# Performance work log

Hardware: AMD Instinct MI355X
Metric: run time of the kernel (lower is better)

Reference implementation:

```python
import jax, jax.numpy as jnp
import numpy as np

H = 16        # attention heads
KVH = 4       # kv heads (GQA)
D = 128       # qk head_dim = qk_nope(64) + qk_rope(64)
ROPE = 64     # rotary sub-dim
VCH = 128     # v_channels
HID = 2048    # hidden size
E = 8         # routed experts
K = 2         # top-k
EPS = 1e-6
THETA = 10000.0


def rmsnorm(x, w):
    return x * jax.lax.rsqrt(jnp.mean(x * x, axis=-1, keepdims=True) + EPS) * w


def apply_rope(x, pos):
    # x: [T, h, ROPE]; rotate-half convention on the rope sub-dim
    half = ROPE // 2
    inv_freq = 1.0 / (THETA ** (jnp.arange(half, dtype=jnp.float32) / half))
    ang = pos.astype(jnp.float32)[:, None] * inv_freq          # [T, half]
    cos = jnp.cos(ang)[:, None, :]
    sin = jnp.sin(ang)[:, None, :]
    x1, x2 = x[..., :half], x[..., half:]
    return jnp.concatenate([x1 * cos - x2 * sin, x1 * sin + x2 * cos], axis=-1)


def swiglu(x, w_gate, w_up, w_down):
    return (jax.nn.silu(x @ w_gate) * (x @ w_up)) @ w_down


def setup_inputs() -> dict:
    key = jax.random.key(0)
    ks = jax.random.split(key, 16)
    T = 2048
    sc = 0.02
    n = lambda k, s: jax.random.normal(k, s, dtype=jnp.float32) * sc
    return {
        "x": jax.random.normal(ks[0], (T, HID), dtype=jnp.float32),
        "positions": jnp.arange(T, dtype=jnp.int32),
        "ln1_w": jnp.ones((HID,), jnp.float32),
        "qkv_w": n(ks[1], (HID, H * D + KVH * D + KVH * VCH)),
        "qkv_b": n(ks[2], (H * D + KVH * D + KVH * VCH,)),
        "k_ln_w": jnp.ones((D,), jnp.float32),
        "o_w": n(ks[3], (H * VCH, HID)),
        "ln2_w": jnp.ones((HID,), jnp.float32),
        "router_w": n(ks[4], (HID, E)),
        "w1": n(ks[5], (E, HID, 512)),
        "w2": n(ks[6], (E, 512, HID)),
        "w3": n(ks[7], (E, HID, 512)),
        "sw1": n(ks[8], (HID, 1024)),
        "sw2": n(ks[9], (1024, HID)),
        "sw3": n(ks[10], (HID, 1024)),
    }


def reference(x, positions, ln1_w, qkv_w, qkv_b, k_ln_w, o_w, ln2_w,
              router_w, w1, w2, w3, sw1, sw2, sw3):
    T = x.shape[0]
    # --- attention block ---
    h = rmsnorm(x, ln1_w)
    qkv = h @ qkv_w + qkv_b
    q = qkv[:, : H * D].reshape(T, H, D)
    k = qkv[:, H * D : H * D + KVH * D].reshape(T, KVH, D)
    v = qkv[:, H * D + KVH * D :].reshape(T, KVH, VCH)
    k = rmsnorm(k, k_ln_w)  # per-head k_layernorm over head_dim
    # rope applied to the trailing qk_rope_dim of q/k
    q = jnp.concatenate([q[..., : D - ROPE], apply_rope(q[..., D - ROPE :], positions)], -1)
    k = jnp.concatenate([k[..., : D - ROPE], apply_rope(k[..., D - ROPE :], positions)], -1)
    rep = H // KVH
    kf = jnp.repeat(k, rep, axis=1)   # [T, H, D]
    vf = jnp.repeat(v, rep, axis=1)   # [T, H, VCH]
    scale = D ** -0.5
    scores = jnp.einsum("qhd,khd->hqk", q, kf) * scale
    causal = jnp.tril(jnp.ones((T, T), dtype=bool))
    scores = jnp.where(causal[None], scores, jnp.float32(-1e30))
    p = jax.nn.softmax(scores, axis=-1)
    attn = jnp.einsum("hqk,khv->qhv", p, vf).reshape(T, H * VCH)
    x = x + attn @ o_w
    # --- MoE block: shared expert + top-k routed experts ---
    h2 = rmsnorm(x, ln2_w)
    probs = jax.nn.softmax(h2 @ router_w, axis=-1)            # [T, E]
    topw, topi = jax.lax.top_k(probs, K)
    topw = topw / jnp.sum(topw, axis=-1, keepdims=True)        # renormalize top-k
    combine = jnp.sum(jax.nn.one_hot(topi, E, dtype=h2.dtype) * topw[..., None], axis=1)  # [T, E]
    moe = swiglu(h2, sw1, sw3, sw2)                            # shared expert
    for e in range(E):  # small fixed expert count
        moe = moe + combine[:, e : e + 1] * swiglu(h2, w1[e], w3[e], w2[e])
    return x + moe
```

## Files before the change

### kernel.cpp

```cpp
#include <hip/hip_runtime.h>


typedef _Float16 half_t;
typedef _Float16 half8 __attribute__((ext_vector_type(8)));
typedef _Float16 half2v __attribute__((ext_vector_type(2)));
typedef float    f32x4 __attribute__((ext_vector_type(4)));
typedef float    floatx4 __attribute__((ext_vector_type(4)));

#define T_TOK 2048
#define HIDN  2048
#define NH    16
#define NKVH  4
#define HD    128
#define QKV_N 3072
#define NEXP  8
#define NPAIR_MAX 4608

#define MFMA16(a,b,c) __builtin_amdgcn_mfma_f32_16x16x32_f16(a,b,c,0,0,0)

__device__ __forceinline__ void gload_lds16(const half_t* g, half_t* l) {
    __builtin_amdgcn_global_load_lds(
        (const __attribute__((address_space(1))) void*)g,
        (__attribute__((address_space(3))) void*)l, 16, 0, 0);
}

__device__ __forceinline__ float silu_f(float g) {
    return g / (1.0f + expf(-g));
}

__global__ __launch_bounds__(256)
void rmsnorm_split_k(const float* __restrict__ x, const float* __restrict__ w,
                     half_t* __restrict__ hi, half_t* __restrict__ lo)
{
    const int row = blockIdx.x, tid = threadIdx.x;
    const float* xr = x + (size_t)row * HIDN;
    floatx4 v0 = *(const floatx4*)(xr + tid * 8);
    floatx4 v1 = *(const floatx4*)(xr + tid * 8 + 4);
    float ss = v0[0]*v0[0] + v0[1]*v0[1] + v0[2]*v0[2] + v0[3]*v0[3]
             + v1[0]*v1[0] + v1[1]*v1[1] + v1[2]*v1[2] + v1[3]*v1[3];
    for (int o = 32; o; o >>= 1) ss += __shfl_down(ss, o);
    __shared__ float red[4];
    if ((tid & 63) == 0) red[tid >> 6] = ss;
    __syncthreads();
    ss = red[0] + red[1] + red[2] + red[3];
    float rs = rsqrtf(ss * (1.0f / HIDN) + 1e-6f);
    floatx4 w0 = *(const floatx4*)(w + tid * 8);
    floatx4 w1 = *(const floatx4*)(w + tid * 8 + 4);
    float vv[8] = { v0[0]*w0[0], v0[1]*w0[1], v0[2]*w0[2], v0[3]*w0[3],
                    v1[0]*w1[0], v1[1]*w1[1], v1[2]*w1[2], v1[3]*w1[3] };
    half8 hv, lv;
#pragma unroll
    for (int j = 0; j < 8; ++j) {
        float o = vv[j] * rs;
        half_t h = (half_t)o;
        hv[j] = h;
        lv[j] = (half_t)((o - (float)h) * 1024.0f);
    }
    *(half8*)(hi + (size_t)row * HIDN + tid * 8) = hv;
    if (lo) *(half8*)(lo + (size_t)row * HIDN + tid * 8) = lv;
}

__global__ __launch_bounds__(256)
void transpose_split2(const float* __restrict__ src,
                      half_t* __restrict__ dh, half_t* __restrict__ dl,
                      int sstride, int dstride)
{
    __shared__ float tile[32][36];
    const int n0 = blockIdx.x * 32, k0 = blockIdx.y * 32;
    const int tid = threadIdx.x;
    {
        int r = tid >> 3, c = (tid & 7) * 4;
        *(floatx4*)&tile[r][c] =
            *(const floatx4*)(src + (size_t)(k0 + r) * sstride + n0 + c);
    }
    __syncthreads();
    int n = tid & 31, g = tid >> 5, gg = g & 3;
    half8 hv;
    if (g < 4) {
#pragma unroll
        for (int j = 0; j < 8; ++j) hv[j] = (half_t)tile[gg * 8 + j][n];
        *(half8*)(dh + (size_t)(n0 + n) * dstride + k0 + gg * 8) = hv;
    } else {
#pragma unroll
        for (int j = 0; j < 8; ++j) {
            float v = tile[gg * 8 + j][n];
            half_t h = (half_t)v;
            hv[j] = (half_t)((v - (float)h) * 1024.0f);
        }
        *(half8*)(dl + (size_t)(n0 + n) * dstride + k0 + gg * 8) = hv;
    }
}

__global__ __launch_bounds__(256)
void transpose_f16(const float* __restrict__ src, half_t* __restrict__ dh,
                   int sstride, int dstride)
{
    __shared__ float tile[32][68];
    const int n0 = blockIdx.x * 64, k0 = blockIdx.y * 32;
    const int tid = threadIdx.x;
    {
        int r = tid >> 3, c = (tid & 7) * 4;
        const float* s = src + (size_t)(k0 + r) * sstride + n0;
        *(floatx4*)&tile[r][c]      = *(const floatx4*)(s + c);
        *(floatx4*)&tile[r][c + 32] = *(const floatx4*)(s + c + 32);
    }
    __syncthreads();
    int n = tid & 63, g = tid >> 6;
    half8 hv;
#pragma unroll
    for (int j = 0; j < 8; ++j) hv[j] = (half_t)tile[g * 8 + j][n];
    *(half8*)(dh + (size_t)(n0 + n) * dstride + k0 + g * 8) = hv;
}

__global__ __launch_bounds__(256)
void vt_transpose_perm(const float* __restrict__ src, half_t* __restrict__ dh)
{
    __shared__ float tile[32][68];
    const int n0 = blockIdx.x * 64, k0 = blockIdx.y * 32;
    const int tid = threadIdx.x;
    {
        int r = tid >> 3, c = (tid & 7) * 4;
        const float* s = src + (size_t)(k0 + r) * QKV_N + n0;
        *(floatx4*)&tile[r][c]      = *(const floatx4*)(s + c);
        *(floatx4*)&tile[r][c + 32] = *(const floatx4*)(s + c + 32);
    }
    __syncthreads();
    int n = tid & 63, g = tid >> 6;
    half8 hv;
#pragma unroll
    for (int tt = 0; tt < 8; ++tt) {
        int c_src = (tt & 1) * 16 + 4 * g + (tt >> 1);
        hv[tt] = (half_t)tile[c_src][n];
    }
    *(half8*)(dh + (size_t)(n0 + n) * T_TOK + k0 + g * 8) = hv;
}

__global__ __launch_bounds__(256)
void w13_transpose(const float* __restrict__ sw1, const float* __restrict__ w1,
                   const float* __restrict__ sw3, const float* __restrict__ w3,
                   half_t* __restrict__ dst)
{
    __shared__ float tile[32][68];
    const int n0 = blockIdx.x * 64, k0 = blockIdx.y * 32;
    const int tid = threadIdx.x;
    const float* base;
    int stride;
    if (n0 < 1024)      { base = sw1 + n0; stride = 1024; }
    else if (n0 < 2048) { base = sw3 + (n0 - 1024); stride = 1024; }
    else if (n0 < 6144) { int e = (n0 - 2048) >> 9;
                          base = w1 + (size_t)e * HIDN * 512 + ((n0 - 2048) & 511);
                          stride = 512; }
    else                { int e = (n0 - 6144) >> 9;
                          base = w3 + (size_t)e * HIDN * 512 + ((n0 - 6144) & 511);
                          stride = 512; }
    {
        int r = tid >> 3, c = (tid & 7) * 4;
        const float* s = base + (size_t)(k0 + r) * stride;
        *(floatx4*)&tile[r][c]      = *(const floatx4*)(s + c);
        *(floatx4*)&tile[r][c + 32] = *(const floatx4*)(s + c + 32);
    }
    __syncthreads();
    int n = tid & 63, g = tid >> 6;
    half8 hv;
#pragma unroll
    for (int j = 0; j < 8; ++j) hv[j] = (half_t)tile[g * 8 + j][n];
    *(half8*)(dst + (size_t)(n0 + n) * HIDN + k0 + g * 8) = hv;
}

__global__ __launch_bounds__(256)
void w2_transpose(const float* __restrict__ sw2, const float* __restrict__ w2,
                  half_t* __restrict__ dst)
{
    __shared__ float tile[32][68];
    const int n0 = blockIdx.x * 64, k0 = blockIdx.y * 32;
    const int tid = threadIdx.x;
    {
        int r = tid >> 3, c = (tid & 7) * 4;
        int k = k0 + r;
        const float* s;
        if (k < 1024) s = sw2 + (size_t)k * HIDN + n0;
        else {
            int e = (k - 1024) >> 9, kk = (k - 1024) & 511;
            s = w2 + ((size_t)e * 512 + kk) * HIDN + n0;
        }
        *(floatx4*)&tile[r][c]      = *(const floatx4*)(s + c);
        *(floatx4*)&tile[r][c + 32] = *(const floatx4*)(s + c + 32);
    }
    __syncthreads();
    int n = tid & 63, g = tid >> 6;
    half8 hv;
#pragma unroll
    for (int j = 0; j < 8; ++j) hv[j] = (half_t)tile[g * 8 + j][n];
    *(half8*)(dst + (size_t)(n0 + n) * 5120 + k0 + g * 8) = hv;
}

__global__ __launch_bounds__(256)
void owu_kernel(const float* __restrict__ ow, const float* __restrict__ ln2w,
                const float* __restrict__ rw, float* __restrict__ owu,
                int* __restrict__ cnt, int* __restrict__ pairTok,
                float* __restrict__ pairW)
{
    if (blockIdx.x < 18) {
        int idx = blockIdx.x * 256 + threadIdx.x;
        if (idx < NPAIR_MAX) { pairTok[idx] = 0; pairW[idx] = 0.0f; }
        if (idx < NEXP) cnt[idx] = 0;
    }
    const int k = blockIdx.x * 4 + (threadIdx.x >> 6);
    const int lane = threadIdx.x & 63;
    float acc[NEXP] = {};
    const float* row = ow + (size_t)k * HIDN;
#pragma unroll
    for (int j = 0; j < 8; ++j) {
        int c = j * 256 + lane * 4;
        floatx4 ov = *(const floatx4*)(row + c);
        floatx4 lw = *(const floatx4*)(ln2w + c);
#pragma unroll
        for (int i = 0; i < 4; ++i) {
            float s = ov[i] * lw[i];
            const float* rwc = rw + (size_t)(c + i) * NEXP;
#pragma unroll
            for (int e = 0; e < NEXP; ++e) acc[e] += s * rwc[e];
        }
    }
#pragma unroll
    for (int e = 0; e < NEXP; ++e)
        for (int o = 32; o; o >>= 1) acc[e] += __shfl_down(acc[e], o);
    if (lane == 0) {
#pragma unroll
        for (int e = 0; e < NEXP; ++e) owu[(size_t)k * NEXP + e] = acc[e];
    }
}

__global__ __launch_bounds__(256)
void z_kernel(const float* __restrict__ qkv, const float* __restrict__ owu,
              half_t* __restrict__ zt)
{
    const int kv = blockIdx.x, tid = threadIdx.x;
    const int hh = tid >> 4, li = tid & 15;
    const float* vrow = qkv + (size_t)kv * QKV_N + 2560 + (hh >> 2) * HD;
    const int d0 = li * 8;
    float acc[NEXP] = {};
#pragma unroll
    for (int j = 0; j < 8; ++j) {
        float v = vrow[d0 + j];
        const float* ou = owu + (size_t)(hh * HD + d0 + j) * NEXP;
#pragma unroll
        for (int e = 0; e < NEXP; ++e) acc[e] += v * ou[e];
    }
#pragma unroll
    for (int e = 0; e < NEXP; ++e)
        for (int o = 1; o < 16; o <<= 1) acc[e] += __shfl_xor(acc[e], o);
    if (li == 0) {
        int j = kv & 31;
        int s = ((j & 15) << 1) | (j >> 4);
        size_t base = (size_t)(kv & ~31) + s;
#pragma unroll
        for (int e = 0; e < NEXP; ++e)
            zt[(size_t)(hh * 8 + e) * T_TOK + base] = (half_t)acc[e];
    }
}

template<bool SPLIT, int BM>
__global__ __launch_bounds__(256, 2)
void gemm_f16(const half_t* __restrict__ Ah, const half_t* __restrict__ Al,
              const half_t* __restrict__ Bth, const half_t* __restrict__ Btl,
              const float* __restrict__ bias, const float* __restrict__ res,
              float* __restrict__ Cf, half_t* __restrict__ Ch,
              int M, int N, int K, int lda, int ldb)
{
    constexpr int NBUF = SPLIT ? 2 : 1;
    constexpr int MR = BM / 32;
    __shared__ half_t As[2][NBUF][BM * 32];
    __shared__ half_t Bs[2][NBUF][128 * 32];
    const int tid = threadIdx.x, lane = tid & 63, wid = tid >> 6;
    const int l15 = lane & 15, l4 = lane >> 4;
    const int row0 = blockIdx.y * BM, col0 = blockIdx.x * 128;
    const int wr = (wid >> 1) * (BM / 2), wc = (wid & 1) * 64;
    f32x4 accM[MR][4] = {}, accC[MR][4] = {};
    const int lrw = lane >> 2, lcl = (lane & 3) * 8;

#define STAGE(BUF, K0)                                                        \
    do {                                                                      \
        _Pragma("unroll")                                                     \
        for (int j = 0; j < BM / 64; ++j) {                                   \
            const int r = wid * (BM / 4) + j * 16;                            \
            const size_t ga = (size_t)(row0 + r + lrw) * lda + (K0) + lcl;    \
            gload_lds16(Ah + ga, &As[BUF][0][r * 32]);                        \
            if constexpr (SPLIT) gload_lds16(Al + ga, &As[BUF][1][r * 32]);   \
        }                                                                     \
        _Pragma("unroll")                                                     \
        for (int j = 0; j < 2; ++j) {                                         \
            const int r = wid * 32 + j * 16;                                  \
            const size_t gb = (size_t)(col0 + r + lrw) * ldb + (K0) + lcl;    \
            gload_lds16(Bth + gb, &Bs[BUF][0][r * 32]);                       \
            if constexpr (SPLIT) gload_lds16(Btl + gb, &Bs[BUF][1][r * 32]);  \
        }                                                                     \
    } while (0)

    STAGE(0, 0);
    __syncthreads();
    int cur = 0;
    for (int k0 = 0; k0 < K; k0 += 32, cur ^= 1) {
        if (k0 + 32 < K) STAGE(cur ^ 1, k0 + 32);
        half8 ah[MR], al[MR], bh[4], bl[4];
#pragma unroll
        for (int m = 0; m < MR; ++m) {
            int off = (wr + m * 16 + l15) * 32 + l4 * 8;
            ah[m] = *(const half8*)&As[cur][0][off];
            if constexpr (SPLIT) al[m] = *(const half8*)&As[cur][1][off];
        }
#pragma unroll
        for (int n = 0; n < 4; ++n) {
            int off = (wc + n * 16 + l15) * 32 + l4 * 8;
            bh[n] = *(const half8*)&Bs[cur][0][off];
            if constexpr (SPLIT) bl[n] = *(const half8*)&Bs[cur][1][off];
        }
#pragma unroll
        for (int m = 0; m < MR; ++m)
#pragma unroll
            for (int n = 0; n < 4; ++n) {
                accM[m][n] = MFMA16(ah[m], bh[n], accM[m][n]);
                if constexpr (SPLIT) {
                    accC[m][n] = MFMA16(ah[m], bl[n], accC[m][n]);
                    accC[m][n] = MFMA16(al[m], bh[n], accC[m][n]);
                }
            }
        __syncthreads();
    }
#undef STAGE

#pragma unroll
    for (int m = 0; m < MR; ++m) {
#pragma unroll
        for (int n = 0; n < 4; ++n) {
            int gr0 = row0 + wr + m * 16 + l4 * 4;
            int gc  = col0 + wc + n * 16 + l15;
            float b = bias ? bias[gc] : 0.0f;
#pragma unroll
            for (int i = 0; i < 4; ++i) {
                float v = accM[m][n][i];
                if constexpr (SPLIT) v += accC[m][n][i] * (1.0f / 1024.0f);
                v += b;
                size_t idx = (size_t)(gr0 + i) * N + gc;
                if (res) v += res[idx];
                if (Cf) Cf[idx] = v;
                if (Ch) Ch[idx] = (half_t)v;
            }
        }
    }
}

__global__ __launch_bounds__(256, 2)
void gemm_gu_all(const half_t* __restrict__ h2, const half_t* __restrict__ W13t,
                 const int* __restrict__ pairTok, const int* __restrict__ basep,
                 const float* __restrict__ pairW,
                 half_t* __restrict__ As_out, half_t* __restrict__ Ab_out)
{
    __shared__ union SM {
        struct { half_t As[2][64 * 32]; half_t Bs[2][128 * 32]; } s;
        half_t ex[64][136];
    } sm;
    const int bid = blockIdx.x;
    const bool grouped = (bid >= 512);
    int ct, row0;
    if (!grouped) { ct = bid & 15;          row0 = (bid >> 4) * 64; }
    else          { int g = bid - 512; ct = g & 7; row0 = (g >> 3) * 64; }
    const int tid = threadIdx.x, lane = tid & 63, wid = tid >> 6;
    const int l15 = lane & 15, l4 = lane >> 4;
    const int lrw = lane >> 2, lcl = (lane & 3) * 8;
    int gbase, ubase;
    if (grouped) {
        int e = 0;
#pragma unroll
        for (int i = 1; i < NEXP; ++i) if (row0 >= basep[i]) e = i;
        gbase = 2048 + 512 * e + ct * 64;
        ubase = 6144 + 512 * e + ct * 64;
    } else {
        gbase = ct * 64;
        ubase = 1024 + ct * 64;
    }
    const int wr = (wid >> 1) * 32, wc = (wid & 1) * 64;
    const half_t* Abase;
    if (grouped) {
        const int tok = pairTok[row0 + wid * 16 + lrw];
        Abase = h2 + (size_t)tok * HIDN + lcl;
    } else {
        Abase = h2 + (size_t)(row0 + wid * 16 + lrw) * HIDN + lcl;
    }
    f32x4 acc[2][4] = {};

#define GSTAGE(BUF, K0)                                                       \
    do {                                                                      \
        gload_lds16(Abase + (K0), &sm.s.As[BUF][(wid * 16) * 32]);            \
        _Pragma("unroll")                                                     \
        for (int j = 0; j < 2; ++j) {                                         \
            const int r = wid * 32 + j * 16;                                  \
            const int grow = (r < 64) ? gbase + r : ubase + (r - 64);         \
            const size_t gb = (size_t)(grow + lrw) * HIDN + (K0) + lcl;       \
            gload_lds16(W13t + gb, &sm.s.Bs[BUF][r * 32]);                    \
        }                                                                     \
    } while (0)

    GSTAGE(0, 0);
    __syncthreads();
    int cur = 0;
    for (int k0 = 0; k0 < HIDN; k0 += 32, cur ^= 1) {
        if (k0 + 32 < HIDN) GSTAGE(cur ^ 1, k0 + 32);
        half8 ah[2], bh[4];
#pragma unroll
        for (int m = 0; m < 2; ++m)
            ah[m] = *(const half8*)&sm.s.As[cur][(wr + m * 16 + l15) * 32 + l4 * 8];
#pragma unroll
        for (int n = 0; n < 4; ++n)
            bh[n] = *(const half8*)&sm.s.Bs[cur][(wc + n * 16 + l15) * 32 + l4 * 8];
#pragma unroll
        for (int m = 0; m < 2; ++m)
#pragma unroll
            for (int n = 0; n < 4; ++n)
                acc[m][n] = MFMA16(ah[m], bh[n], acc[m][n]);
        __syncthreads();
    }
#undef GSTAGE

#pragma unroll
    for (int m = 0; m < 2; ++m)
#pragma unroll
        for (int n = 0; n < 4; ++n)
#pragma unroll
            for (int i = 0; i < 4; ++i)
                sm.ex[wr + m * 16 + l4 * 4 + i][wc + n * 16 + l15] =
                    (half_t)acc[m][n][i];
    __syncthreads();
    const int OSTR = grouped ? 512 : 1024;
    half_t* outp = grouped ? Ab_out : As_out;
#pragma unroll
    for (int w2 = 0; w2 < 2; ++w2) {
        int unit = tid * 2 + w2;
        int row = unit >> 3, cgx = (unit & 7) * 8;
        half8 g8 = *(const half8*)&sm.ex[row][cgx];
        half8 u8 = *(const half8*)&sm.ex[row][64 + cgx];
        float wgt = grouped ? pairW[row0 + row] : 1.0f;
        half8 o8;
#pragma unroll
        for (int j = 0; j < 8; ++j)
            o8[j] = (half_t)(silu_f((float)g8[j]) * (float)u8[j] * wgt);
        *(half8*)(outp + (size_t)(row0 + row) * OSTR + ct * 64 + cgx) = o8;
    }
}

__global__ __launch_bounds__(256, 2)
void gemm_down_all(const half_t* __restrict__ As_sh, const half_t* __restrict__ Ab,
                   const half_t* __restrict__ W2t, const int* __restrict__ basep,
                   const float* __restrict__ x2, float* __restrict__ out,
                   half_t* __restrict__ Ypair)
{
    __shared__ half_t Asm[2][64 * 32];
    __shared__ half_t Bsm[2][128 * 32];
    const int tid = threadIdx.x, lane = tid & 63, wid = tid >> 6;
    const int l15 = lane & 15, l4 = lane >> 4;
    const int lrw = lane >> 2, lcl = (lane & 3) * 8;
    const int col0 = blockIdx.x * 128;
    const bool shared = (blockIdx.y < 32);
    const int row0 = (shared ? blockIdx.y : blockIdx.y - 32) * 64;
    const half_t* A;
    int lda, K, bcol;
    if (shared) { A = As_sh; lda = 1024; K = 1024; bcol = 0; }
    else {
        int e = 0;
#pragma unroll
        for (int i = 1; i < NEXP; ++i) if (row0 >= basep[i]) e = i;
        A = Ab; lda = 512; K = 512; bcol = 1024 + 512 * e;
    }
    const int wr = (wid >> 1) * 32, wc = (wid & 1) * 64;
    f32x4 acc[2][4] = {};

#define DSTAGE(BUF, K0)                                                       \
    do {                                                                      \
        const size_t ga = (size_t)(row0 + wid * 16 + lrw) * lda + (K0) + lcl; \
        gload_lds16(A + ga, &Asm[BUF][(wid * 16) * 32]);                      \
        _Pragma("unroll")                                                     \
        for (int j = 0; j < 2; ++j) {                                         \
            const int r = wid * 32 + j * 16;                                  \
            const size_t gb = (size_t)(col0 + r + lrw) * 5120 + bcol + (K0) + lcl; \
            gload_lds16(W2t + gb, &Bsm[BUF][r * 32]);                         \
        }                                                                     \
    } while (0)

    DSTAGE(0, 0);
    __syncthreads();
    int cur = 0;
    for (int k0 = 0; k0 < K; k0 += 32, cur ^= 1) {
        if (k0 + 32 < K) DSTAGE(cur ^ 1, k0 + 32);
        half8 ah[2], bh[4];
#pragma unroll
        for (int m = 0; m < 2; ++m)
            ah[m] = *(const half8*)&Asm[cur][(wr + m * 16 + l15) * 32 + l4 * 8];
#pragma unroll
        for (int n = 0; n < 4; ++n)
            bh[n] = *(const half8*)&Bsm[cur][(wc + n * 16 + l15) * 32 + l4 * 8];
#pragma unroll
        for (int m = 0; m < 2; ++m)
#pragma unroll
            for (int n = 0; n < 4; ++n)
                acc[m][n] = MFMA16(ah[m], bh[n], acc[m][n]);
        __syncthreads();
    }
#undef DSTAGE

#pragma unroll
    for (int m = 0; m < 2; ++m)
#pragma unroll
        for (int n = 0; n < 4; ++n) {
            int gr0 = row0 + wr + m * 16 + l4 * 4;
            int gc  = col0 + wc + n * 16 + l15;
#pragma unroll
            for (int i = 0; i < 4; ++i) {
                size_t idx = (size_t)(gr0 + i) * HIDN + gc;
                if (shared) out[idx] = x2[idx] + acc[m][n][i];
                else        Ypair[idx] = (half_t)acc[m][n][i];
            }
        }
}

__global__ __launch_bounds__(256)
void qkv_prep(const float* __restrict__ qkv, const int* __restrict__ pos,
              const float* __restrict__ klnw,
              half_t* __restrict__ qh, half_t* __restrict__ ql,
              half_t* __restrict__ kh, half_t* __restrict__ kl)
{
    const int t = blockIdx.x, tid = threadIdx.x, lane = tid & 63, wid = tid >> 6;
    const float* row = qkv + (size_t)t * QKV_N;
    __shared__ float cs[32], sn[32];
    if (tid < 32) {
        double freq = exp((double)tid * -0.28782313662425572);
        double ang = (double)pos[t] * freq;
        const double twopi = 6.283185307179586476925286766559;
        ang -= twopi * floor(ang * (1.0 / twopi));
        float a = (float)ang;
        cs[tid] = cosf(a);
        sn[tid] = sinf(a);
    }
    __syncthreads();

    const float qscale = 0.08838834764831845f;
    {
        const int hh = tid >> 4, d0 = (tid & 15) * 8;
        const float* qrow = row + hh * HD;
        float outv[8];
        if (d0 < 64) {
#pragma unroll
            for (int j = 0; j < 8; ++j) outv[j] = qrow[d0 + j];
        } else if (d0 < 96) {
            int j0 = d0 - 64;
#pragma unroll
            for (int j = 0; j < 8; ++j) {
                int jj = j0 + j;
                outv[j] = qrow[64 + jj] * cs[jj] - qrow[96 + jj] * sn[jj];
            }
        } else {
            int j0 = d0 - 96;
#pragma unroll
            for (int j = 0; j < 8; ++j) {
                int jj = j0 + j;
                outv[j] = qrow[64 + jj] * sn[jj] + qrow[96 + jj] * cs[jj];
            }
        }
        half8 hv, lv;
#pragma unroll
        for (int j = 0; j < 8; ++j) {
            float o = outv[j] * qscale;
            half_t h = (half_t)o;
            hv[j] = h;
            lv[j] = (half_t)((o - (float)h) * 1024.0f);
        }
        size_t base = (size_t)t * (NH * HD) + hh * HD + d0;
        *(half8*)(qh + base) = hv;
        *(half8*)(ql + base) = lv;
    }
    {
        const float* krow = row + NH * HD + wid * HD;
        float a0 = krow[lane], a1 = krow[64 + lane];
        float ss = a0 * a0 + a1 * a1;
        for (int o = 32; o; o >>= 1) ss += __shfl_down(ss, o);
        ss = __shfl(ss, 0);
        float rs = rsqrtf(ss * (1.0f / HD) + 1e-6f);
        float n0 = a0 * rs * klnw[lane];
        float n1 = a1 * rs * klnw[64 + lane];
        float other = __shfl_xor(n1, 32);
        int j = lane & 31;
        float o1 = (lane < 32) ? (n1 * cs[j] - other * sn[j])
                               : (other * sn[j] + n1 * cs[j]);
        size_t base = (size_t)t * (NKVH * HD) + wid * HD;
        half_t h;
        h = (half_t)n0; kh[base + lane] = h;
        kl[base + lane] = (half_t)((n0 - (float)h) * 1024.0f);
        h = (half_t)o1; kh[base + 64 + lane] = h;
        kl[base + 64 + lane] = (half_t)((o1 - (float)h) * 1024.0f);
    }
}

__global__ __launch_bounds__(256, 2)
void attn_kernel(const half_t* __restrict__ qh, const half_t* __restrict__ ql,
                 const half_t* __restrict__ kh, const half_t* __restrict__ kl,
                 const half_t* __restrict__ vth, const half_t* __restrict__ zt,
                 half_t* __restrict__ oh,
                 float* __restrict__ Op0, float* __restrict__ Op1,
                 float* __restrict__ Op2, float* __restrict__ ml,
                 float* __restrict__ zpart, float* __restrict__ zfin)
{
    const int bid = blockIdx.x;
    const int h = bid & 15;
    int rrem = bid >> 4, q = 31, nch = 6, c = 0;
    for (; q >= 0; --q) {
        nch = (q + 6) / 6;
        if (rrem < nch) { c = rrem; break; }
        rrem -= nch;
    }
    const int nt = q + 1;
    const int kvbeg = ((c * nt) / nch) * 64;
    const int kvend = (((c + 1) * nt) / nch) * 64;

    const int kvh = h >> 2;
    const int tid = threadIdx.x, lane = tid & 63, wid = tid >> 6;
    const int q0 = q * 64 + wid * 16;
    const int l15 = lane & 15, l4 = lane >> 4;

    __shared__ half_t Ksh[64][136], Ksl[64][136];
    __shared__ half_t Vsh[144][72];
    __shared__ half_t Ph[4][16][72];

    half8 qfh[4], qfl[4];
    {
        const size_t qb = (size_t)(q0 + l15) * (NH * HD) + h * HD + l4 * 8;
#pragma unroll
        for (int cc = 0; cc < 4; ++cc) {
            qfh[cc] = *(const half8*)(qh + qb + cc * 32);
            qfl[cc] = *(const half8*)(ql + qb + cc * 32);
        }
    }

    f32x4 om[9] = {};
    float mrow[4] = { -1e30f, -1e30f, -1e30f, -1e30f };
    float lrow[4] = {};

    const int kr = tid >> 2, kc0 = (tid & 3) * 32;
    const int vd = tid >> 1, vc0 = (tid & 1) * 32;
    const int ze = tid >> 5, zc0 = (tid & 31) * 2;
    uint4 rkh0, rkh1, rkh2, rkh3, rkl0, rkl1, rkl2, rkl3;
    uint4 rv0, rv1, rv2, rv3;
    unsigned rzw;

#define LOAD_TILE(KV0)                                                        \
    do {                                                                      \
        size_t sk = (size_t)((KV0) + kr) * (NKVH * HD) + kvh * HD + kc0;      \
        rkh0 = *(const uint4*)(kh + sk);       rkl0 = *(const uint4*)(kl + sk);      \
        rkh1 = *(const uint4*)(kh + sk + 8);   rkl1 = *(const uint4*)(kl + sk + 8);  \
        rkh2 = *(const uint4*)(kh + sk + 16);  rkl2 = *(const uint4*)(kl + sk + 16); \
        rkh3 = *(const uint4*)(kh + sk + 24);  rkl3 = *(const uint4*)(kl + sk + 24); \
        size_t sv = (size_t)(kvh * HD + vd) * T_TOK + (KV0) + vc0;            \
        rv0 = *(const uint4*)(vth + sv);       rv1 = *(const uint4*)(vth + sv + 8);  \
        rv2 = *(const uint4*)(vth + sv + 16);  rv3 = *(const uint4*)(vth + sv + 24); \
        rzw = *(const unsigned*)(zt + (size_t)(h * 8 + ze) * T_TOK + (KV0) + zc0);   \
    } while (0)

    LOAD_TILE(kvbeg);
    for (int kv0 = kvbeg; kv0 < kvend; kv0 += 64) {
        *(uint4*)&Ksh[kr][kc0]      = rkh0;  *(uint4*)&Ksl[kr][kc0]      = rkl0;
        *(uint4*)&Ksh[kr][kc0 + 8]  = rkh1;  *(uint4*)&Ksl[kr][kc0 + 8]  = rkl1;
        *(uint4*)&Ksh[kr][kc0 + 16] = rkh2;  *(uint4*)&Ksl[kr][kc0 + 16] = rkl2;
        *(uint4*)&Ksh[kr][kc0 + 24] = rkh3;  *(uint4*)&Ksl[kr][kc0 + 24] = rkl3;
        *(uint4*)&Vsh[vd][vc0]      = rv0;   *(uint4*)&Vsh[vd][vc0 + 8]  = rv1;
        *(uint4*)&Vsh[vd][vc0 + 16] = rv2;   *(uint4*)&Vsh[vd][vc0 + 24] = rv3;
        *(unsigned*)&Vsh[128 + ze][zc0] = rzw;
        __syncthreads();
        if (kv0 + 64 < kvend) LOAD_TILE(kv0 + 64);

        f32x4 sf[4];
        __builtin_amdgcn_s_setprio(1);
#pragma unroll
        for (int t2 = 0; t2 < 4; ++t2) {
            f32x4 s = {}, sc1 = {}, sc2 = {};
#pragma unroll
            for (int cc = 0; cc < 4; ++cc) {
                half8 bh = *(const half8*)&Ksh[t2 * 16 + l15][cc * 32 + l4 * 8];
                half8 bl = *(const half8*)&Ksl[t2 * 16 + l15][cc * 32 + l4 * 8];
                s   = MFMA16(qfh[cc], bh, s);
                sc1 = MFMA16(qfh[cc], bl, sc1);
                sc2 = MFMA16(qfl[cc], bh, sc2);
            }
            sf[t2] = s + (sc1 + sc2) * (1.0f / 1024.0f);
        }
        __builtin_amdgcn_s_setprio(0);

        float pmax[4];
#pragma unroll
        for (int i = 0; i < 4; ++i) {
            const int qg = q0 + l4 * 4 + i;
#pragma unroll
            for (int t2 = 0; t2 < 4; ++t2) {
                int kvg = kv0 + t2 * 16 + l15;
                if (kvg > qg) sf[t2][i] = -1e30f;
            }
            float mx = fmaxf(fmaxf(sf[0][i], sf[1][i]),
                             fmaxf(sf[2][i], sf[3][i]));
#pragma unroll
            for (int o = 1; o < 16; o <<= 1) mx = fmaxf(mx, __shfl_xor(mx, o));
            pmax[i] = mx;
        }
        float dm = fmaxf(fmaxf(pmax[0] - mrow[0], pmax[1] - mrow[1]),
                         fmaxf(pmax[2] - mrow[2], pmax[3] - mrow[3]));
        if (__any(dm > 6.0f)) {
#pragma unroll
            for (int i = 0; i < 4; ++i) {
                float mnew = fmaxf(mrow[i], pmax[i]);
                float resc = expf(mrow[i] - mnew);
                lrow[i] *= resc;
#pragma unroll
                for (int c8 = 0; c8 < 9; ++c8) om[c8][i] *= resc;
                mrow[i] = mnew;
            }
        }
#pragma unroll
        for (int i = 0; i < 4; ++i) {
            float p0 = expf(sf[0][i] - mrow[i]);
            float p1 = expf(sf[1][i] - mrow[i]);
            float p2 = expf(sf[2][i] - mrow[i]);
            float p3 = expf(sf[3][i] - mrow[i]);
            lrow[i] += (p0 + p1) + (p2 + p3);
            half2v ppA = { (half_t)p0, (half_t)p1 };
            half2v ppB = { (half_t)p2, (half_t)p3 };
            *(half2v*)&Ph[wid][l4 * 4 + i][l15 * 2]      = ppA;
            *(half2v*)&Ph[wid][l4 * 4 + i][32 + l15 * 2] = ppB;
        }

        half8 pa0 = *(const half8*)&Ph[wid][l15][l4 * 8];
        half8 pa1 = *(const half8*)&Ph[wid][l15][32 + l4 * 8];
        __builtin_amdgcn_s_setprio(1);
#pragma unroll
        for (int c8 = 0; c8 < 9; ++c8) {
            half8 v0 = *(const half8*)&Vsh[c8 * 16 + l15][l4 * 8];
            half8 v1 = *(const half8*)&Vsh[c8 * 16 + l15][32 + l4 * 8];
            om[c8] = MFMA16(pa0, v0, om[c8]);
            om[c8] = MFMA16(pa1, v1, om[c8]);
        }
        __builtin_amdgcn_s_setprio(0);
        __syncthreads();
    }
#undef LOAD_TILE

#pragma unroll
    for (int i = 0; i < 4; ++i)
#pragma unroll
        for (int o = 1; o < 16; o <<= 1) lrow[i] += __shfl_xor(lrow[i], o);

    if (l15 < 8) {
        const int e = l15;
#pragma unroll
        for (int i = 0; i < 4; ++i) {
            int row64 = wid * 16 + l4 * 4 + i;
            if (nch == 1) {
                zfin[((size_t)(q * 64 + row64) * 16 + h) * 8 + e] =
                    om[8][i] / lrow[i];
            } else {
                zpart[((size_t)bid * 64 + row64) * 8 + e] = om[8][i];
            }
        }
    }

    if (nch == 1) {
#pragma unroll
        for (int c8 = 0; c8 < 8; ++c8) {
#pragma unroll
            for (int i = 0; i < 4; ++i) {
                float v = om[c8][i] / lrow[i];
                size_t idx = (size_t)(q0 + l4 * 4 + i) * (NH * HD) + h * HD
                           + c8 * 16 + l15;
                oh[idx] = (half_t)v;
            }
        }
    } else {
        float* Op = (bid < 768)  ? Op0 + (size_t)bid * 8192
                  : (bid < 1280) ? Op1 + (size_t)(bid - 768) * 8192
                                 : Op2 + (size_t)(bid - 1280) * 8192;
#pragma unroll
        for (int c8 = 0; c8 < 8; ++c8) {
#pragma unroll
            for (int i = 0; i < 4; ++i) {
                int row64 = wid * 16 + l4 * 4 + i;
                Op[row64 * 128 + c8 * 16 + l15] = om[c8][i];
            }
        }
        if (l15 == 0) {
#pragma unroll
            for (int i = 0; i < 4; ++i) {
                int row64 = wid * 16 + l4 * 4 + i;
                ml[(size_t)bid * 128 + row64]      = mrow[i];
                ml[(size_t)bid * 128 + 64 + row64] = lrow[i];
            }
        }
    }
}

__device__ __forceinline__ const float* slot_ptr(int s, const float* Op0,
                                                 const float* Op1,
                                                 const float* Op2)
{
    return (s < 768)  ? Op0 + (size_t)s * 8192
         : (s < 1280) ? Op1 + (size_t)(s - 768) * 8192
                      : Op2 + (size_t)(s - 1280) * 8192;
}

__global__ __launch_bounds__(256)
void attn_combine(const float* __restrict__ Op0, const float* __restrict__ Op1,
                  const float* __restrict__ Op2, const float* __restrict__ ml,
                  const float* __restrict__ zpart,
                  half_t* __restrict__ oh, float* __restrict__ zfin)
{
    const int bid = blockIdx.x;
    const int h = bid & 15, q = 6 + (bid >> 4);
    const int nch = (q + 6) / 6;
    int r0 = 0;
    for (int j = 31; j > q; --j) r0 += (j + 6) / 6;
    const int tid = threadIdx.x;
    const int row = tid >> 2, cg = (tid & 3) * 32;

    float M = -1e30f;
    for (int c = 0; c < nch; ++c) {
        int s = (r0 + c) * 16 + h;
        M = fmaxf(M, ml[(size_t)s * 128 + row]);
    }
    float wsum = 0.0f;
    for (int c = 0; c < nch; ++c) {
        int s = (r0 + c) * 16 + h;
        wsum += ml[(size_t)s * 128 + 64 + row] *
                expf(ml[(size_t)s * 128 + row] - M);
    }
    float inv = 1.0f / wsum;

    if ((tid & 3) == 0) {
        f32x4 a = {0,0,0,0}, b = {0,0,0,0};
        for (int c = 0; c < nch; ++c) {
            int s = (r0 + c) * 16 + h;
            float w = expf(ml[(size_t)s * 128 + row] - M) * inv;
            size_t zo = ((size_t)s * 64 + row) * 8;
            a += w * (*(const f32x4*)&zpart[zo]);
            b += w * (*(const f32x4*)&zpart[zo + 4]);
        }
        size_t zo = ((size_t)(q * 64 + row) * 16 + h) * 8;
        *(f32x4*)&zfin[zo]     = a;
        *(f32x4*)&zfin[zo + 4] = b;
    }

    size_t obase = (size_t)(q * 64 + row) * (NH * HD) + h * HD + cg;
#pragma unroll
    for (int jj = 0; jj < 4; ++jj) {
        floatx4 a0 = {0,0,0,0}, a1 = {0,0,0,0};
        for (int c = 0; c < nch; ++c) {
            int s = (r0 + c) * 16 + h;
            float w = expf(ml[(size_t)s * 128 + row] - M) * inv;
            const float* base = slot_ptr(s, Op0, Op1, Op2) + row * 128 + cg;
            a0 += w * (*(const floatx4*)(base + jj * 8));
            a1 += w * (*(const floatx4*)(base + jj * 8 + 4));
        }
        half8 hv;
#pragma unroll
        for (int k = 0; k < 4; ++k) {
            hv[k]     = (half_t)a0[k];
            hv[4 + k] = (half_t)a1[k];
        }
        *(half8*)(oh + obase + jj * 8) = hv;
    }
}

__global__ __launch_bounds__(256)
void router_linear(const float* __restrict__ x, const float* __restrict__ zfin,
                   const float* __restrict__ x2,
                   const float* __restrict__ ln2w, const float* __restrict__ rw,
                   int* __restrict__ topi, float* __restrict__ topv,
                   int* __restrict__ cnt, half_t* __restrict__ h2)
{
    const int t = blockIdx.x, tid = threadIdx.x;
    const float* xr2 = x2 + (size_t)t * HIDN + tid * 8;
    floatx4 x2a = *(const floatx4*)(xr2);
    floatx4 x2b = *(const floatx4*)(xr2 + 4);
    float ss = x2a[0]*x2a[0] + x2a[1]*x2a[1] + x2a[2]*x2a[2] + x2a[3]*x2a[3]
             + x2b[0]*x2b[0] + x2b[1]*x2b[1] + x2b[2]*x2b[2] + x2b[3]*x2b[3];
    for (int o = 32; o; o >>= 1) ss += __shfl_down(ss, o);
    __shared__ float red[4];
    if ((tid & 63) == 0) red[tid >> 6] = ss;
    __syncthreads();
    ss = red[0] + red[1] + red[2] + red[3];
    float rs = rsqrtf(ss * (1.0f / HIDN) + 1e-6f);

    const float* xr = x + (size_t)t * HIDN + tid * 8;
    floatx4 xa = *(const floatx4*)(xr);
    floatx4 xb = *(const floatx4*)(xr + 4);
    floatx4 lwa = *(const floatx4*)(ln2w + tid * 8);
    floatx4 lwb = *(const floatx4*)(ln2w + tid * 8 + 4);

    float acc[NEXP] = {};
#pragma unroll
    for (int j = 0; j < 8; ++j) {
        int c = tid * 8 + j;
        float xv = (j < 4 ? xa[j] : xb[j - 4]) * (j < 4 ? lwa[j] : lwb[j - 4]);
        const float* rwc = rw + (size_t)c * NEXP;
#pragma unroll
        for (int e = 0; e < NEXP; ++e) acc[e] += xv * rwc[e];
    }
#pragma unroll
    for (int e = 0; e < NEXP; ++e)
        for (int o = 32; o; o >>= 1) acc[e] += __shfl_down(acc[e], o);
    __shared__ float red8[4][NEXP];
    if ((tid & 63) == 0)
#pragma unroll
        for (int e = 0; e < NEXP; ++e) red8[tid >> 6][e] = acc[e];

    __shared__ float zred[NEXP * 16];
    if (tid < 128) {
        int hh = tid >> 3, e = tid & 7;
        zred[e * 16 + hh] = zfin[((size_t)t * 16 + hh) * 8 + e];
    }

    half8 h2v;
#pragma unroll
    for (int j = 0; j < 8; ++j) {
        float xv = (j < 4 ? x2a[j] : x2b[j - 4]) * (j < 4 ? lwa[j] : lwb[j - 4]);
        h2v[j] = (half_t)(xv * rs);
    }
    *(half8*)(h2 + (size_t)t * HIDN + tid * 8) = h2v;

    __syncthreads();
    if (tid == 0) {
        float lg[NEXP];
#pragma unroll
        for (int e = 0; e < NEXP; ++e) {
            float zs = 0.0f;
#pragma unroll
            for (int hh = 0; hh < 16; ++hh) zs += zred[e * 16 + hh];
            lg[e] = (red8[0][e] + red8[1][e] + red8[2][e] + red8[3][e] + zs) * rs;
        }
        int i1 = 0;
        for (int e = 1; e < NEXP; ++e) if (lg[e] > lg[i1]) i1 = e;
        int i2 = (i1 == 0) ? 1 : 0;
        for (int e = 0; e < NEXP; ++e) if (e != i1 && lg[e] > lg[i2]) i2 = e;
        float mx = lg[i1];
        float p1 = expf(lg[i1] - mx), p2 = expf(lg[i2] - mx);
        float inv = 1.0f / (p1 + p2);
        topi[2 * t] = i1;       topi[2 * t + 1] = i2;
        topv[2 * t] = p1 * inv; topv[2 * t + 1] = p2 * inv;
        atomicAdd(&cnt[i1], 1);
        atomicAdd(&cnt[i2], 1);
    }
}

__global__ __launch_bounds__(256)
void moe_build(const int* __restrict__ cnt, int* __restrict__ basep,
               const int* __restrict__ topi, const float* __restrict__ topv,
               int* __restrict__ pairTok, float* __restrict__ pairW,
               int* __restrict__ pairPos)
{
    const int e = blockIdx.x;
    int base = 0;
    for (int i = 0; i < e; ++i) base += (cnt[i] + 63) & ~63;
    if (threadIdx.x == 0) basep[e] = base;

    const int tid = threadIdx.x, lane = tid & 63, wv = tid >> 6;
    __shared__ int wsum[4];
    int run = base;
    for (int i0 = 0; i0 < 2 * T_TOK; i0 += 256) {
        int i = i0 + tid;
        bool m = (topi[i] == e);
        unsigned long long bal = __ballot(m);
        int lpre = __popcll(bal & ((1ull << lane) - 1ull));
        if (lane == 0) wsum[wv] = (int)__popcll(bal);
        __syncthreads();
        int woff = 0;
        for (int w = 0; w < wv; ++w) woff += wsum[w];
        if (m) {
            int pos = run + woff + lpre;
            pairTok[pos] = i >> 1;
            pairW[pos]   = topv[i];
            pairPos[i]   = pos;
        }
        run += wsum[0] + wsum[1] + wsum[2] + wsum[3];
        __syncthreads();
    }
}

__global__ __launch_bounds__(256)
void moe_final(const half_t* __restrict__ Ypair, const int* __restrict__ pairPos,
               float* __restrict__ out)
{
    int t = blockIdx.x, c0 = threadIdx.x * 8;
    int p1 = pairPos[2 * t], p2 = pairPos[2 * t + 1];
    half8 y1 = *(const half8*)(Ypair + (size_t)p1 * HIDN + c0);
    half8 y2 = *(const half8*)(Ypair + (size_t)p2 * HIDN + c0);
    float* o = out + (size_t)t * HIDN + c0;
    floatx4 a = *(floatx4*)o, b = *(floatx4*)(o + 4);
#pragma unroll
    for (int j = 0; j < 4; ++j) {
        a[j] += (float)y1[j] + (float)y2[j];
        b[j] += (float)y1[4 + j] + (float)y2[4 + j];
    }
    *(floatx4*)o = a;
    *(floatx4*)(o + 4) = b;
}

extern "C" void kernel_launch(void* const* d_in, const int* in_sizes, int n_in,
                              void* d_out, int out_size, void* d_ws, size_t ws_size,
                              hipStream_t stream)
{
    (void)in_sizes; (void)n_in; (void)out_size; (void)ws_size;
    const float* x    = (const float*)d_in[0];
    const int*   pos  = (const int*)  d_in[1];
    const float* ln1w = (const float*)d_in[2];
    const float* qkvw = (const float*)d_in[3];
    const float* qkvb = (const float*)d_in[4];
    const float* klnw = (const float*)d_in[5];
    const float* ow   = (const float*)d_in[6];
    const float* ln2w = (const float*)d_in[7];
    const float* rw   = (const float*)d_in[8];
    const float* w1   = (const float*)d_in[9];
    const float* w2   = (const float*)d_in[10];
    const float* w3   = (const float*)d_in[11];
    const float* sw1  = (const float*)d_in[12];
    const float* sw2  = (const float*)d_in[13];
    const float* sw3  = (const float*)d_in[14];
    float* out = (float*)d_out;

    char* ws = (char*)d_ws;
    const size_t AB = 16842752;
    float*  x2      = (float*)(ws);
    half_t* h_hi    = (half_t*)(ws + AB);
    half_t* h_lo    = (half_t*)(ws + AB + 8388608);
    half_t* qkvwt_h = (half_t*)(ws + AB + 16777216);
    half_t* qkvwt_l = (half_t*)(ws + AB + 29360128);
    float*  qkv     = (float*)(ws + AB + 41943040);
    half_t* q_h     = (half_t*)(ws + AB + 67108864);
    half_t* q_l     = (half_t*)(ws + AB + 75497472);
    half_t* k_h     = (half_t*)(ws + AB + 83886080);
    half_t* k_l     = (half_t*)(ws + AB + 85983232);
    half_t* vt_h    = (half_t*)(ws + AB + 88080384);
    half_t* attn_h  = (half_t*)(ws + AB);
    half_t* zt      = (half_t*)(ws + AB + 8388608);
    half_t* owt     = (half_t*)(ws + AB + 16777216);
    float*  ow_u    = (float*)(ws + AB + 25165824);
    float*  mlpart  = (float*)(ws + AB + 25231360);
    float*  Opart0  = (float*)(ws + AB + 41943040);
    float*  Opart1  = (float*)(ws);
    float*  Opart2  = (float*)(ws + AB + 29360128);
    half_t* h2      = (half_t*)(ws + AB + 33554432);
    half_t* W13t    = (half_t*)(ws + AB + 41943040);
    half_t* As_sh   = (half_t*)(ws + AB);
    half_t* Ab      = (half_t*)(ws + AB + 16777216);
    half_t* W2t     = (half_t*)(ws + AB + 41943040);
    half_t* Ypair   = (half_t*)(ws + AB + 92274688);

    char* meta = ws + (size_t)(AB + 117440512);
    int*    cnt     = (int*)  (meta + 0);
    int*    basep   = (int*)  (meta + 128);
    int*    topi    = (int*)  (meta + 256);
    float*  topv    = (float*)(meta + 16640);
    int*    pairPos = (int*)  (meta + 33024);
    int*    pairTok = (int*)  (meta + 49408);
    float*  pairW   = (float*)(meta + 67840);
    float*  zpart   = (float*)(meta + 131072);
    float*  zfin    = (float*)(meta + 131072 + 3342336);

    dim3 b256(256);

    rmsnorm_split_k<<<T_TOK, b256, 0, stream>>>(x, ln1w, h_hi, h_lo);
    transpose_split2<<<dim3(QKV_N / 32, HIDN / 32), b256, 0, stream>>>(
        qkvw, qkvwt_h, qkvwt_l, QKV_N, HIDN);
    gemm_f16<true, 128><<<dim3(QKV_N / 128, T_TOK / 128), b256, 0, stream>>>(
        h_hi, h_lo, qkvwt_h, qkvwt_l, qkvb, nullptr, qkv, nullptr,
        T_TOK, QKV_N, HIDN, HIDN, HIDN);
    qkv_prep<<<T_TOK, b256, 0, stream>>>(qkv, pos, klnw, q_h, q_l, k_h, k_l);
    vt_transpose_perm<<<dim3(512 / 64, T_TOK / 32), b256, 0, stream>>>(
        qkv + 2560, vt_h);
    transpose_f16<<<dim3(HIDN / 64, HIDN / 32), b256, 0, stream>>>(
        ow, owt, HIDN, HIDN);
    owu_kernel<<<512, b256, 0, stream>>>(ow, ln2w, rw, ow_u,
                                         cnt, pairTok, pairW);
    z_kernel<<<T_TOK, b256, 0, stream>>>(qkv, ow_u, zt);
    attn_kernel<<<1632, b256, 0, stream>>>(
        q_h, q_l, k_h, k_l, vt_h, zt, attn_h,
        Opart0, Opart1, Opart2, mlpart, zpart, zfin);
    attn_combine<<<416, b256, 0, stream>>>(Opart0, Opart1, Opart2, mlpart,
                                           zpart, attn_h, zfin);
    gemm_f16<false, 128><<<dim3(HIDN / 128, T_TOK / 128), b256, 0, stream>>>(
        attn_h, nullptr, owt, nullptr, nullptr, x, x2, nullptr,
        T_TOK, HIDN, HIDN, HIDN, HIDN);
    router_linear<<<T_TOK, b256, 0, stream>>>(
        x, zfin, x2, ln2w, rw, topi, topv, cnt, h2);
    moe_build<<<NEXP, b256, 0, stream>>>(cnt, basep, topi, topv,
                                         pairTok, pairW, pairPos);
    w13_transpose<<<dim3(10240 / 64, HIDN / 32), b256, 0, stream>>>(
        sw1, w1, sw3, w3, W13t);
    gemm_gu_all<<<512 + 8 * (NPAIR_MAX / 64), b256, 0, stream>>>(
        h2, W13t, pairTok, basep, pairW, As_sh, Ab);
    w2_transpose<<<dim3(HIDN / 64, 5120 / 32), b256, 0, stream>>>(sw2, w2, W2t);
    gemm_down_all<<<dim3(16, 104), b256, 0, stream>>>(
        As_sh, Ab, W2t, basep, x2, out, Ypair);
    moe_final<<<T_TOK, b256, 0, stream>>>(Ypair, pairPos, out);
}
```

Measured before the change: 579.4 us.

## Enlarge attention query tile to 128 rows and store split-KV partials in fp16

The attention kernel now runs 512-thread blocks of 8 waves that cover 128 query rows. Each K/V tile loaded into LDS is therefore reused by twice as many queries, and the split-KV chunk schedule and block count are recomputed for the new tiling. Partial outputs for the split chunks are written as fp16 instead of fp32, and the combine kernel is adapted to read them, which cuts partial-buffer traffic at some cost in accuracy. The tighter launch bound of 512 threads with 4 blocks per CU caps registers per thread and may cause spills, while LDS use per block limits how many blocks actually fit.

After: 675.7 us. 1.17x slower.

```diff
diff --git a/kernel.cpp b/kernel.cpp
--- a/kernel.cpp
+++ b/kernel.cpp
@@ -599,35 +599,35 @@
     }
 }
 
-__global__ __launch_bounds__(256, 2)
+__global__ __launch_bounds__(512, 4)
 void attn_kernel(const half_t* __restrict__ qh, const half_t* __restrict__ ql,
                  const half_t* __restrict__ kh, const half_t* __restrict__ kl,
                  const half_t* __restrict__ vth, const half_t* __restrict__ zt,
                  half_t* __restrict__ oh,
-                 float* __restrict__ Op0, float* __restrict__ Op1,
-                 float* __restrict__ Op2, float* __restrict__ ml,
+                 half_t* __restrict__ Op0, half_t* __restrict__ Op1,
+                 float* __restrict__ ml,
                  float* __restrict__ zpart, float* __restrict__ zfin)
 {
     const int bid = blockIdx.x;
     const int h = bid & 15;
-    int rrem = bid >> 4, q = 31, nch = 6, c = 0;
+    int rrem = bid >> 4, q = 15, nch = 7, c = 0;
     for (; q >= 0; --q) {
-        nch = (q + 6) / 6;
+        nch = (2 * (q + 1) + 4) / 5;
         if (rrem < nch) { c = rrem; break; }
         rrem -= nch;
     }
-    const int nt = q + 1;
+    const int nt = 2 * (q + 1);
     const int kvbeg = ((c * nt) / nch) * 64;
     const int kvend = (((c + 1) * nt) / nch) * 64;
 
     const int kvh = h >> 2;
     const int tid = threadIdx.x, lane = tid & 63, wid = tid >> 6;
-    const int q0 = q * 64 + wid * 16;
+    const int q0 = q * 128 + wid * 16;
     const int l15 = lane & 15, l4 = lane >> 4;
 
     __shared__ half_t Ksh[64][136], Ksl[64][136];
     __shared__ half_t Vsh[144][72];
-    __shared__ half_t Ph[4][16][72];
+    __shared__ half_t Ph[8][16][72];
 
     half8 qfh[4], qfl[4];
     {
@@ -643,35 +643,29 @@
     float mrow[4] = { -1e30f, -1e30f, -1e30f, -1e30f };
     float lrow[4] = {};
 
-    const int kr = tid >> 2, kc0 = (tid & 3) * 32;
-    const int vd = tid >> 1, vc0 = (tid & 1) * 32;
+    const int kr = tid >> 3, kc0 = (tid & 7) * 16;
+    const int vd = tid >> 2, vc0 = (tid & 3) * 16;
     const int ze = tid >> 5, zc0 = (tid & 31) * 2;
-    uint4 rkh0, rkh1, rkh2, rkh3, rkl0, rkl1, rkl2, rkl3;
-    uint4 rv0, rv1, rv2, rv3;
+    uint4 rkh0, rkh1, rkl0, rkl1, rv0, rv1;
     unsigned rzw;
 
 #define LOAD_TILE(KV0)                                                        \
     do {                                                                      \
         size_t sk = (size_t)((KV0) + kr) * (NKVH * HD) + kvh * HD + kc0;      \
-        rkh0 = *(const uint4*)(kh + sk);       rkl0 = *(const uint4*)(kl + sk);      \
-        rkh1 = *(const uint4*)(kh + sk + 8);   rkl1 = *(const uint4*)(kl + sk + 8);  \
-        rkh2 = *(const uint4*)(kh + sk + 16);  rkl2 = *(const uint4*)(kl + sk + 16); \
-        rkh3 = *(const uint4*)(kh + sk + 24);  rkl3 = *(const uint4*)(kl + sk + 24); \
+        rkh0 = *(const uint4*)(kh + sk);   rkh1 = *(const uint4*)(kh + sk + 8); \
+        rkl0 = *(const uint4*)(kl + sk);   rkl1 = *(const uint4*)(kl + sk + 8); \
         size_t sv = (size_t)(kvh * HD + vd) * T_TOK + (KV0) + vc0;            \
-        rv0 = *(const uint4*)(vth + sv);       rv1 = *(const uint4*)(vth + sv + 8);  \
-        rv2 = *(const uint4*)(vth + sv + 16);  rv3 = *(const uint4*)(vth + sv + 24); \
-        rzw = *(const unsigned*)(zt + (size_t)(h * 8 + ze) * T_TOK + (KV0) + zc0);   \
+        rv0 = *(const uint4*)(vth + sv);   rv1 = *(const uint4*)(vth + sv + 8); \
+        if (tid < 256)                                                        \
+            rzw = *(const unsigned*)(zt + (size_t)(h * 8 + ze) * T_TOK + (KV0) + zc0); \
     } while (0)
 
     LOAD_TILE(kvbeg);
     for (int kv0 = kvbeg; kv0 < kvend; kv0 += 64) {
-        *(uint4*)&Ksh[kr][kc0]      = rkh0;  *(uint4*)&Ksl[kr][kc0]      = rkl0;
-        *(uint4*)&Ksh[kr][kc0 + 8]  = rkh1;  *(uint4*)&Ksl[kr][kc0 + 8]  = rkl1;
-        *(uint4*)&Ksh[kr][kc0 + 16] = rkh2;  *(uint4*)&Ksl[kr][kc0 + 16] = rkl2;
-        *(uint4*)&Ksh[kr][kc0 + 24] = rkh3;  *(uint4*)&Ksl[kr][kc0 + 24] = rkl3;
-        *(uint4*)&Vsh[vd][vc0]      = rv0;   *(uint4*)&Vsh[vd][vc0 + 8]  = rv1;
-        *(uint4*)&Vsh[vd][vc0 + 16] = rv2;   *(uint4*)&Vsh[vd][vc0 + 24] = rv3;
-        *(unsigned*)&Vsh[128 + ze][zc0] = rzw;
+        *(uint4*)&Ksh[kr][kc0]     = rkh0;  *(uint4*)&Ksh[kr][kc0 + 8] = rkh1;
+        *(uint4*)&Ksl[kr][kc0]     = rkl0;  *(uint4*)&Ksl[kr][kc0 + 8] = rkl1;
+        *(uint4*)&Vsh[vd][vc0]     = rv0;   *(uint4*)&Vsh[vd][vc0 + 8] = rv1;
+        if (tid < 256) *(unsigned*)&Vsh[128 + ze][zc0] = rzw;
         __syncthreads();
         if (kv0 + 64 < kvend) LOAD_TILE(kv0 + 64);
 
@@ -757,12 +751,12 @@
         const int e = l15;
 #pragma unroll
         for (int i = 0; i < 4; ++i) {
-            int row64 = wid * 16 + l4 * 4 + i;
+            int row128 = wid * 16 + l4 * 4 + i;
             if (nch == 1) {
-                zfin[((size_t)(q * 64 + row64) * 16 + h) * 8 + e] =
+                zfin[((size_t)(q * 128 + row128) * 16 + h) * 8 + e] =
                     om[8][i] / lrow[i];
             } else {
-                zpart[((size_t)bid * 64 + row64) * 8 + e] = om[8][i];
+                zpart[((size_t)bid * 128 + row128) * 8 + e] = om[8][i];
             }
         }
     }
@@ -779,96 +773,95 @@
             }
         }
     } else {
-        float* Op = (bid < 768)  ? Op0 + (size_t)bid * 8192
-                  : (bid < 1280) ? Op1 + (size_t)(bid - 768) * 8192
-                                 : Op2 + (size_t)(bid - 1280) * 8192;
+        half_t* Op = (bid < 768) ? Op0 + (size_t)bid * 16384
+                                 : Op1 + (size_t)(bid - 768) * 16384;
 #pragma unroll
         for (int c8 = 0; c8 < 8; ++c8) {
 #pragma unroll
             for (int i = 0; i < 4; ++i) {
-                int row64 = wid * 16 + l4 * 4 + i;
-                Op[row64 * 128 + c8 * 16 + l15] = om[c8][i];
+                int row128 = wid * 16 + l4 * 4 + i;
+                Op[row128 * 128 + c8 * 16 + l15] = (half_t)om[c8][i];
             }
         }
         if (l15 == 0) {
 #pragma unroll
             for (int i = 0; i < 4; ++i) {
-                int row64 = wid * 16 + l4 * 4 + i;
-                ml[(size_t)bid * 128 + row64]      = mrow[i];
-                ml[(size_t)bid * 128 + 64 + row64] = lrow[i];
-            }
-        }
-    }
-}
-
-__device__ __forceinline__ const float* slot_ptr(int s, const float* Op0,
-                                                 const float* Op1,
-                                                 const float* Op2)
-{
-    return (s < 768)  ? Op0 + (size_t)s * 8192
-         : (s < 1280) ? Op1 + (size_t)(s - 768) * 8192
-                      : Op2 + (size_t)(s - 1280) * 8192;
-}
-
-__global__ __launch_bounds__(256)
-void attn_combine(const float* __restrict__ Op0, const float* __restrict__ Op1,
-                  const float* __restrict__ Op2, const float* __restrict__ ml,
-                  const float* __restrict__ zpart,
+                int row128 = wid * 16 + l4 * 4 + i;
+                ml[(size_t)bid * 256 + row128]       = mrow[i];
+                ml[(size_t)bid * 256 + 128 + row128] = lrow[i];
+            }
+        }
+    }
+}
+
+__device__ __forceinline__ const half_t* slot_ptr(int s, const half_t* Op0,
+                                                  const half_t* Op1)
+{
+    return (s < 768) ? Op0 + (size_t)s * 16384
+                     : Op1 + (size_t)(s - 768) * 16384;
+}
+
+__global__ __launch_bounds__(256)
+void attn_combine(const half_t* __restrict__ Op0, const half_t* __restrict__ Op1,
+                  const float* __restrict__ ml, const float* __restrict__ zpart,
                   half_t* __restrict__ oh, float* __restrict__ zfin)
 {
     const int bid = blockIdx.x;
-    const int h = bid & 15, q = 6 + (bid >> 4);
-    const int nch = (q + 6) / 6;
+    const int h = bid & 15, qi = 2 + (bid >> 4);
+    const int nch = (2 * (qi + 1) + 4) / 5;
     int r0 = 0;
-    for (int j = 31; j > q; --j) r0 += (j + 6) / 6;
+    for (int j = 15; j > qi; --j) r0 += (2 * (j + 1) + 4) / 5;
     const int tid = threadIdx.x;
-    const int row = tid >> 2, cg = (tid & 3) * 32;
-
-    float M = -1e30f;
-    for (int c = 0; c < nch; ++c) {
-        int s = (r0 + c) * 16 + h;
-        M = fmaxf(M, ml[(size_t)s * 128 + row]);
-    }
-    float wsum = 0.0f;
-    for (int c = 0; c < nch; ++c) {
-        int s = (r0 + c) * 16 + h;
-        wsum += ml[(size_t)s * 128 + 64 + row] *
-                expf(ml[(size_t)s * 128 + row] - M);
-    }
-    float inv = 1.0f / wsum;
-
-    if ((tid & 3) == 0) {
-        f32x4 a = {0,0,0,0}, b = {0,0,0,0};
+
+#pragma unroll
+    for (int rp = 0; rp < 2; ++rp) {
+        const int row = rp * 64 + (tid >> 2), cg = (tid & 3) * 32;
+
+        float M = -1e30f;
         for (int c = 0; c < nch; ++c) {
             int s = (r0 + c) * 16 + h;
-            float w = expf(ml[(size_t)s * 128 + row] - M) * inv;
-            size_t zo = ((size_t)s * 64 + row) * 8;
-            a += w * (*(const f32x4*)&zpart[zo]);
-            b += w * (*(const f32x4*)&zpart[zo + 4]);
-        }
-        size_t zo = ((size_t)(q * 64 + row) * 16 + h) * 8;
-        *(f32x4*)&zfin[zo]     = a;
-        *(f32x4*)&zfin[zo + 4] = b;
-    }
-
-    size_t obase = (size_t)(q * 64 + row) * (NH * HD) + h * HD + cg;
-#pragma unroll
-    for (int jj = 0; jj < 4; ++jj) {
-        floatx4 a0 = {0,0,0,0}, a1 = {0,0,0,0};
+            M = fmaxf(M, ml[(size_t)s * 256 + row]);
+        }
+        float wsum = 0.0f;
         for (int c = 0; c < nch; ++c) {
             int s = (r0 + c) * 16 + h;
-            float w = expf(ml[(size_t)s * 128 + row] - M) * inv;
-            const float* base = slot_ptr(s, Op0, Op1, Op2) + row * 128 + cg;
-            a0 += w * (*(const floatx4*)(base + jj * 8));
-            a1 += w * (*(const floatx4*)(base + jj * 8 + 4));
-        }
-        half8 hv;
-#pragma unroll
-        for (int k = 0; k < 4; ++k) {
-            hv[k]     = (half_t)a0[k];
-            hv[4 + k] = (half_t)a1[k];
-        }
-        *(half8*)(oh + obase + jj * 8) = hv;
+            wsum += ml[(size_t)s * 256 + 128 + row] *
+                    expf(ml[(size_t)s * 256 + row] - M);
+        }
+        float inv = 1.0f / wsum;
+
+        if ((tid & 3) == 0) {
+            f32x4 a = {0,0,0,0}, b = {0,0,0,0};
+            for (int c = 0; c < nch; ++c) {
+                int s = (r0 + c) * 16 + h;
+                float w = expf(ml[(size_t)s * 256 + row] - M) * inv;
+                size_t zo = ((size_t)s * 128 + row) * 8;
+                a += w * (*(const f32x4*)&zpart[zo]);
+                b += w * (*(const f32x4*)&zpart[zo + 4]);
+            }
+            size_t zo = ((size_t)(qi * 128 + row) * 16 + h) * 8;
+            *(f32x4*)&zfin[zo]     = a;
+            *(f32x4*)&zfin[zo + 4] = b;
+        }
+
+        size_t obase = (size_t)(qi * 128 + row) * (NH * HD) + h * HD + cg;
+#pragma unroll
+        for (int jj = 0; jj < 4; ++jj) {
+            float a0[8] = {};
+            for (int c = 0; c < nch; ++c) {
+                int s = (r0 + c) * 16 + h;
+                float w = expf(ml[(size_t)s * 256 + row] - M) * inv;
+                const half_t* base = slot_ptr(s, Op0, Op1)
+                                   + row * 128 + cg + jj * 8;
+                half8 v = *(const half8*)base;
+#pragma unroll
+                for (int k = 0; k < 8; ++k) a0[k] += w * (float)v[k];
+            }
+            half8 hv;
+#pragma unroll
+            for (int k = 0; k < 8; ++k) hv[k] = (half_t)a0[k];
+            *(half8*)(oh + obase + jj * 8) = hv;
+        }
     }
 }
 
@@ -1046,9 +1039,8 @@
     half_t* owt     = (half_t*)(ws + AB + 16777216);
     float*  ow_u    = (float*)(ws + AB + 25165824);
     float*  mlpart  = (float*)(ws + AB + 25231360);
-    float*  Opart0  = (float*)(ws + AB + 41943040);
-    float*  Opart1  = (float*)(ws);
-    float*  Opart2  = (float*)(ws + AB + 29360128);
+    half_t* Opart0h = (half_t*)(ws + AB + 41943040);
+    half_t* Opart1h = (half_t*)(ws);
     half_t* h2      = (half_t*)(ws + AB + 33554432);
     half_t* W13t    = (half_t*)(ws + AB + 41943040);
     half_t* As_sh   = (half_t*)(ws + AB);
@@ -1065,7 +1057,7 @@
     int*    pairTok = (int*)  (meta + 49408);
     float*  pairW   = (float*)(meta + 67840);
     float*  zpart   = (float*)(meta + 131072);
-    float*  zfin    = (float*)(meta + 131072 + 3342336);
+    float*  zfin    = (float*)(meta + 131072 + 3866624);
 
     dim3 b256(256);
 
@@ -1083,10 +1075,10 @@
     owu_kernel<<<512, b256, 0, stream>>>(ow, ln2w, rw, ow_u,
                                          cnt, pairTok, pairW);
     z_kernel<<<T_TOK, b256, 0, stream>>>(qkv, ow_u, zt);
-    attn_kernel<<<1632, b256, 0, stream>>>(
+    attn_kernel<<<976, dim3(512), 0, stream>>>(
         q_h, q_l, k_h, k_l, vt_h, zt, attn_h,
-        Opart0, Opart1, Opart2, mlpart, zpart, zfin);
-    attn_combine<<<416, b256, 0, stream>>>(Opart0, Opart1, Opart2, mlpart,
+        Opart0h, Opart1h, mlpart, zpart, zfin);
+    attn_combine<<<224, b256, 0, stream>>>(Opart0h, Opart1h, mlpart,
                                            zpart, attn_h, zfin);
     gemm_f16<false, 128><<<dim3(HIDN / 128, T_TOK / 128), b256, 0, stream>>>(
         attn_h, nullptr, owt, nullptr, nullptr, x, x2, nullptr,
```
